# Kernel optimization log

Measured on AMD Instinct MI355X. Metric: run time of the kernel, lower is better.

Reference implementation:

```python
import jax, jax.numpy as jnp
import numpy as np

D_PAIR = 128
C = 128
LN_EPS = 1e-5


def _layernorm(x, w, b):
    m = jnp.mean(x, axis=-1, keepdims=True)
    v = jnp.var(x, axis=-1, keepdims=True)
    return (x - m) * jax.lax.rsqrt(v + LN_EPS) * w + b


def setup_inputs() -> dict:
    key = jax.random.key(0)
    ks = jax.random.split(key, 12)
    B, N = 1, 512
    Z_raw = jax.random.normal(ks[0], (B, N, N, D_PAIR), dtype=jnp.float32)
    Z_mask_row = jnp.ones((B, N, N), dtype=jnp.float32)
    s = 1.0 / np.sqrt(D_PAIR)
    return {
        "Z_raw": Z_raw,
        "Z_mask_row": Z_mask_row,
        "ln1_w": jnp.ones((D_PAIR,), jnp.float32),
        "ln1_b": jnp.zeros((D_PAIR,), jnp.float32),
        "lrp_w": jax.random.normal(ks[1], (2 * C, D_PAIR), jnp.float32) * s,
        "lrp_b": jnp.zeros((2 * C,), jnp.float32),
        "gate_w": jax.random.normal(ks[2], (2 * C, D_PAIR), jnp.float32) * (0.02 * s),
        "gate_b": jnp.ones((2 * C,), jnp.float32),
        "og_w": jax.random.normal(ks[3], (D_PAIR, D_PAIR), jnp.float32) * (0.02 * s),
        "og_b": jnp.ones((D_PAIR,), jnp.float32),
        "ln2_w": jnp.ones((C,), jnp.float32),
        "ln2_b": jnp.zeros((C,), jnp.float32),
        "op_w": jax.random.normal(ks[4], (D_PAIR, D_PAIR), jnp.float32) * (0.02 * s),
        "out_bias": jnp.zeros((D_PAIR,), jnp.float32),
    }


def reference(Z_raw, Z_mask_row, ln1_w, ln1_b, lrp_w, lrp_b, gate_w, gate_b,
              og_w, og_b, ln2_w, ln2_b, op_w, out_bias):
    # Stage 1: norm + gated left/right projections (single chunk since CHUNK_SIZE is None)
    z = _layernorm(Z_raw, ln1_w, ln1_b)                      # [B,N,N,d]
    g = jax.nn.sigmoid(z @ gate_w.T + gate_b)                # [B,N,N,2c]
    proj = (z @ lrp_w.T + lrp_b) * Z_mask_row[..., None] * g  # [B,N,N,2c]
    left, right = jnp.split(proj, 2, axis=-1)                # each [B,N,N,c]
    # Outgoing triangle multiplication: p[b,i,j,c] = sum_k left[b,i,k,c] * right[b,j,k,c]
    tri = jnp.einsum("bikc,bjkc->bijc", left, right)         # [B,N,N,c]
    # Stage 2: output gate on the raw matmul result, norm+proj, bias+gate+residual
    go = jax.nn.sigmoid(tri @ og_w.T + og_b)                 # [B,N,N,d]
    z2 = _layernorm(tri, ln2_w, ln2_b) @ op_w.T              # [B,N,N,d]
    # dropout_mask is all-ones in the source; residual is the matmul output tri
    return tri + go * (z2 + out_bias)
```

## Files before the change

kernel.cpp:

```cpp
#include <hip/hip_runtime.h>

#define NN 512
#define NP (NN*NN)
#define LN_EPS 1e-5f

typedef __attribute__((ext_vector_type(8))) short short8;
typedef __attribute__((ext_vector_type(4))) float float4v;

__device__ __forceinline__ short f2bf(float x){
  union { float f; unsigned u; } un; un.f = x;
  unsigned r = un.u + 0x7fffu + ((un.u >> 16) & 1u);
  return (short)(r >> 16);
}
__device__ __forceinline__ float bf2f(short b){
  union { unsigned u; float f; } un; un.u = ((unsigned)(unsigned short)b) << 16;
  return un.f;
}
__device__ __forceinline__ float sigmoidf_(float x){ return 1.f/(1.f+__expf(-x)); }

__global__ __launch_bounds__(256) void prep_kernel(
    const float* __restrict__ lrpw, const float* __restrict__ gatew,
    const float* __restrict__ ogwf, const float* __restrict__ opwf,
    short* __restrict__ Wpack, short* __restrict__ ogw, short* __restrict__ opw)
{
  int idx = blockIdx.x*256 + threadIdx.x;
  if (idx < 512*128){
    int r = idx >> 7, k = idx & 127, cc = r >> 1;
    float v = (r & 1) ? gatew[cc*128+k] : lrpw[cc*128+k];
    Wpack[idx] = f2bf(v);
  } else if (idx < 512*128 + 128*128) {
    int j = idx - 512*128; ogw[j] = f2bf(ogwf[j]);
  } else {
    int j = idx - 512*128 - 128*128; opw[j] = f2bf(opwf[j]);
  }
}

__global__ __launch_bounds__(512) void stage1_kernel(
    const float* __restrict__ Zraw, const float* __restrict__ mask,
    const float* __restrict__ ln1w, const float* __restrict__ ln1b,
    const float* __restrict__ lrpb, const float* __restrict__ gateb,
    const short* __restrict__ Wpack,
    short* __restrict__ left, short* __restrict__ right)
{
  __shared__ float zraw[64][132];
  __shared__ short zb[64][136];
  __shared__ float part[64][8][2];
  __shared__ float stats[64][2];

  const int t = threadIdx.x;
  const int pos0 = blockIdx.x * 64;

  const float* Zr = Zraw + (size_t)pos0 * 128;
  #pragma unroll
  for (int i = 0; i < 4; i++) {
    int idx = i*512 + t;
    float4v v = *(const float4v*)(Zr + (size_t)idx*4);
    int row = idx >> 5, col = (idx & 31) << 2;
    *(float4v*)&zraw[row][col] = v;
  }
  __syncthreads();

  {
    int pos = t >> 3, seg = t & 7;
    float s = 0.f, ss = 0.f;
    #pragma unroll
    for (int i = 0; i < 16; i++){ float v = zraw[pos][seg*16+i]; s += v; ss += v*v; }
    part[pos][seg][0] = s; part[pos][seg][1] = ss;
  }
  __syncthreads();
  if ((t & 7) == 0) {
    int pos = t >> 3;
    float S = 0.f, SS = 0.f;
    #pragma unroll
    for (int j = 0; j < 8; j++){ S += part[pos][j][0]; SS += part[pos][j][1]; }
    float m = S * (1.f/128.f);
    float v = SS * (1.f/128.f) - m*m;
    stats[pos][0] = m; stats[pos][1] = rsqrtf(v + LN_EPS);
  }
  __syncthreads();
  {
    int pos = t >> 3, seg = t & 7;
    float m = stats[pos][0], r = stats[pos][1];
    #pragma unroll
    for (int i = 0; i < 16; i++){
      int c = seg*16 + i;
      float v = (zraw[pos][c]-m)*r*ln1w[c] + ln1b[c];
      zb[pos][c] = f2bf(v);
    }
  }
  __syncthreads();

  const int w = t >> 6, lane = t & 63;
  const int q = lane >> 4, m15 = lane & 15;

  float4v acc[4][4];
  #pragma unroll
  for (int a = 0; a < 4; a++)
    #pragma unroll
    for (int b = 0; b < 4; b++) acc[a][b] = (float4v){0.f,0.f,0.f,0.f};

  #pragma unroll
  for (int s = 0; s < 4; s++){
    short8 af[4], bfv[4];
    #pragma unroll
    for (int rt = 0; rt < 4; rt++)
      af[rt] = *(const short8*)(Wpack + ((size_t)(w*64 + rt*16 + m15))*128 + s*32 + q*8);
    #pragma unroll
    for (int pt = 0; pt < 4; pt++)
      bfv[pt] = *(const short8*)(&zb[pt*16 + m15][s*32 + q*8]);
    #pragma unroll
    for (int rt = 0; rt < 4; rt++)
      #pragma unroll
      for (int pt = 0; pt < 4; pt++)
        acc[rt][pt] = __builtin_amdgcn_mfma_f32_16x16x32_bf16(af[rt], bfv[pt], acc[rt][pt], 0, 0, 0);
  }

  #pragma unroll
  for (int rt = 0; rt < 4; rt++){
    int rowbase = w*64 + rt*16 + 4*q;
    #pragma unroll
    for (int pt = 0; pt < 4; pt++){
      int pos = pos0 + pt*16 + m15;
      float mk = mask[pos];
      #pragma unroll
      for (int p = 0; p < 2; p++){
        int ch = (rowbase >> 1) + p;
        float lr = acc[rt][pt][2*p]   + lrpb[ch];
        float gt = acc[rt][pt][2*p+1] + gateb[ch];
        float val = lr * mk * sigmoidf_(gt);
        short* dst = (ch < 128) ? (left + (size_t)ch*NP + pos)
                                : (right + (size_t)(ch-128)*NP + pos);
        *dst = f2bf(val);
      }
    }
  }
}

__global__ __launch_bounds__(256) void tri_kernel(
    const short* __restrict__ left, const short* __restrict__ right,
    float* __restrict__ tri)
{
  __shared__ short As[128][72];
  __shared__ short Bs[128][72];

  const int t  = threadIdx.x;
  const int c  = blockIdx.z;
  const int i0 = blockIdx.y * 128;
  const int j0 = blockIdx.x * 128;

  const short* Lp = left  + (size_t)c*NP + (size_t)i0*NN;
  const short* Rp = right + (size_t)c*NP + (size_t)j0*NN;

  const int w = t >> 6, lane = t & 63;
  const int q = lane >> 4, m15 = lane & 15;
  const int wi = w >> 1, wj = w & 1;

  float4v acc[4][4];
  #pragma unroll
  for (int a = 0; a < 4; a++)
    #pragma unroll
    for (int b = 0; b < 4; b++) acc[a][b] = (float4v){0.f,0.f,0.f,0.f};

  for (int it = 0; it < 8; it++){
    const int k0 = it * 64;
    __syncthreads();
    #pragma unroll
    for (int i = 0; i < 4; i++){
      int idx = i*256 + t;
      int row = idx >> 3, c8 = (idx & 7) * 8;
      *(short8*)&As[row][c8] = *(const short8*)(Lp + (size_t)row*NN + k0 + c8);
      *(short8*)&Bs[row][c8] = *(const short8*)(Rp + (size_t)row*NN + k0 + c8);
    }
    __syncthreads();
    #pragma unroll
    for (int s = 0; s < 2; s++){
      short8 af[4], bfv[4];
      #pragma unroll
      for (int mi = 0; mi < 4; mi++)
        af[mi] = *(const short8*)(&As[wi*64 + mi*16 + m15][s*32 + q*8]);
      #pragma unroll
      for (int nj = 0; nj < 4; nj++)
        bfv[nj] = *(const short8*)(&Bs[wj*64 + nj*16 + m15][s*32 + q*8]);
      #pragma unroll
      for (int mi = 0; mi < 4; mi++)
        #pragma unroll
        for (int nj = 0; nj < 4; nj++)
          acc[mi][nj] = __builtin_amdgcn_mfma_f32_16x16x32_bf16(af[mi], bfv[nj], acc[mi][nj], 0, 0, 0);
    }
  }

  float* Tp = tri + (size_t)c*NP;
  #pragma unroll
  for (int mi = 0; mi < 4; mi++)
    #pragma unroll
    for (int nj = 0; nj < 4; nj++)
      #pragma unroll
      for (int r = 0; r < 4; r++){
        int i = i0 + wi*64 + mi*16 + 4*q + r;
        int j = j0 + wj*64 + nj*16 + m15;
        Tp[(size_t)i*NN + j] = acc[mi][nj][r];
      }
}

__global__ __launch_bounds__(256) void stage2_kernel(
    const float* __restrict__ tri,
    const short* __restrict__ ogw, const short* __restrict__ opw,
    const float* __restrict__ ogb, const float* __restrict__ ln2w,
    const float* __restrict__ ln2b, const float* __restrict__ outb,
    float* __restrict__ out)
{
  __shared__ short tb[64][136];
  __shared__ short lnb_s[64][136];
  __shared__ float part[64][4][2];
  __shared__ float stats[64][2];

  const int t = threadIdx.x;
  const int pos0 = blockIdx.x * 64;

  #pragma unroll
  for (int i = 0; i < 8; i++){
    int idx = i*256 + t;
    int cc = idx >> 4, p4 = (idx & 15) << 2;
    float4v v = *(const float4v*)(tri + (size_t)cc*NP + pos0 + p4);
    #pragma unroll
    for (int u = 0; u < 4; u++) tb[p4+u][cc] = f2bf(v[u]);
  }
  __syncthreads();

  {
    int pos = t >> 2, seg = t & 3;
    float s = 0.f, ss = 0.f;
    #pragma unroll
    for (int i = 0; i < 32; i++){ float v = bf2f(tb[pos][seg*32+i]); s += v; ss += v*v; }
    part[pos][seg][0] = s; part[pos][seg][1] = ss;
  }
  __syncthreads();
  if ((t & 3) == 0){
    int pos = t >> 2;
    float S = 0.f, SS = 0.f;
    #pragma unroll
    for (int j = 0; j < 4; j++){ S += part[pos][j][0]; SS += part[pos][j][1]; }
    float m = S * (1.f/128.f);
    float v = SS * (1.f/128.f) - m*m;
    stats[pos][0] = m; stats[pos][1] = rsqrtf(v + LN_EPS);
  }
  __syncthreads();
  {
    int pos = t >> 2, seg = t & 3;
    float m = stats[pos][0], r = stats[pos][1];
    #pragma unroll
    for (int i = 0; i < 32; i++){
      int c = seg*32 + i;
      float v = bf2f(tb[pos][c]);
      lnb_s[pos][c] = f2bf((v-m)*r*ln2w[c] + ln2b[c]);
    }
  }
  __syncthreads();

  const int w = t >> 6, lane = t & 63;
  const int q = lane >> 4, m15 = lane & 15;

  float4v a1[2][4], a2[2][4];
  #pragma unroll
  for (int a = 0; a < 2; a++)
    #pragma unroll
    for (int b = 0; b < 4; b++){ a1[a][b] = (float4v){0.f,0.f,0.f,0.f}; a2[a][b] = (float4v){0.f,0.f,0.f,0.f}; }

  #pragma unroll
  for (int s = 0; s < 4; s++){
    short8 af1[4], af2[4], bv1[2], bv2[2];
    #pragma unroll
    for (int pt = 0; pt < 4; pt++){
      af1[pt] = *(const short8*)(&tb[pt*16 + m15][s*32 + q*8]);
      af2[pt] = *(const short8*)(&lnb_s[pt*16 + m15][s*32 + q*8]);
    }
    #pragma unroll
    for (int dt = 0; dt < 2; dt++){
      int d = w*32 + dt*16 + m15;
      bv1[dt] = *(const short8*)(ogw + (size_t)d*128 + s*32 + q*8);
      bv2[dt] = *(const short8*)(opw + (size_t)d*128 + s*32 + q*8);
    }
    #pragma unroll
    for (int dt = 0; dt < 2; dt++)
      #pragma unroll
      for (int pt = 0; pt < 4; pt++){
        a1[dt][pt] = __builtin_amdgcn_mfma_f32_16x16x32_bf16(af1[pt], bv1[dt], a1[dt][pt], 0, 0, 0);
        a2[dt][pt] = __builtin_amdgcn_mfma_f32_16x16x32_bf16(af2[pt], bv2[dt], a2[dt][pt], 0, 0, 0);
      }
  }

  #pragma unroll
  for (int dt = 0; dt < 2; dt++){
    int d = w*32 + dt*16 + m15;
    float ob = ogb[d], xb = outb[d];
    #pragma unroll
    for (int pt = 0; pt < 4; pt++)
      #pragma unroll
      for (int r = 0; r < 4; r++){
        int pos = pt*16 + 4*q + r;
        float trv = bf2f(tb[pos][d]);
        float go = sigmoidf_(a1[dt][pt][r] + ob);
        float z2 = a2[dt][pt][r] + xb;
        out[(size_t)(pos0+pos)*128 + d] = trv + go*z2;
      }
  }
}

extern "C" void kernel_launch(void* const* d_in, const int* in_sizes, int n_in,
                              void* d_out, int out_size, void* d_ws, size_t ws_size,
                              hipStream_t stream)
{
  const float* Zraw = (const float*)d_in[0];
  const float* mask = (const float*)d_in[1];
  const float* ln1w = (const float*)d_in[2];
  const float* ln1b = (const float*)d_in[3];
  const float* lrpw = (const float*)d_in[4];
  const float* lrpb = (const float*)d_in[5];
  const float* gatew= (const float*)d_in[6];
  const float* gateb= (const float*)d_in[7];
  const float* ogwf = (const float*)d_in[8];
  const float* ogb  = (const float*)d_in[9];
  const float* ln2w = (const float*)d_in[10];
  const float* ln2b = (const float*)d_in[11];
  const float* opwf = (const float*)d_in[12];
  const float* outb = (const float*)d_in[13];
  float* out = (float*)d_out;

  short* left  = (short*)d_ws;
  short* right = left + (size_t)128*NP;
  float* tri   = (float*)(right + (size_t)128*NP);
  short* Wpack = (short*)(tri + (size_t)128*NP);
  short* ogw   = Wpack + 512*128;
  short* opw   = ogw + 128*128;

  hipLaunchKernelGGL(prep_kernel, dim3(384), dim3(256), 0, stream,
                     lrpw, gatew, ogwf, opwf, Wpack, ogw, opw);
  hipLaunchKernelGGL(stage1_kernel, dim3(NP/64), dim3(512), 0, stream,
                     Zraw, mask, ln1w, ln1b, lrpb, gateb, Wpack, left, right);
  hipLaunchKernelGGL(tri_kernel, dim3(4, 4, 128), dim3(256), 0, stream,
                     left, right, tri);
  hipLaunchKernelGGL(stage2_kernel, dim3(NP/64), dim3(256), 0, stream,
                     tri, ogw, opw, ogb, ln2w, ln2b, outb, out);
}
```

Measured before the change: 538.0 us.

## Store tri in bf16, use direct global-to-LDS loads, and register-based layernorms

The triangle matmul output is now stored as bf16 instead of fp32, which halves the write traffic in tri_kernel and the read traffic in stage2. tri_kernel fills shared memory with global_load_lds and an XOR-swizzled layout in place of padding plus register staging. Both layernorms are restructured: stage1 computes its stats in registers with shuffle reductions, and stage2 reads tri per position and reduces through a small shared array, which cuts barriers and shared-memory round trips. The stage2 path already used bf16 for tri, so the extra rounding in storage is minor.

```diff
diff --git a/kernel.cpp b/kernel.cpp
--- a/kernel.cpp
+++ b/kernel.cpp
@@ -17,6 +17,11 @@
   return un.f;
 }
 __device__ __forceinline__ float sigmoidf_(float x){ return 1.f/(1.f+__expf(-x)); }
+
+__device__ __forceinline__ void gl2lds16(const short* g, short* l){
+  __builtin_amdgcn_global_load_lds((const __attribute__((address_space(1))) void*)g,
+                                   (__attribute__((address_space(3))) void*)l, 16, 0, 0);
+}
 
 __global__ __launch_bounds__(256) void prep_kernel(
     const float* __restrict__ lrpw, const float* __restrict__ gatew,
@@ -42,52 +47,43 @@
     const short* __restrict__ Wpack,
     short* __restrict__ left, short* __restrict__ right)
 {
-  __shared__ float zraw[64][132];
   __shared__ short zb[64][136];
-  __shared__ float part[64][8][2];
-  __shared__ float stats[64][2];
 
   const int t = threadIdx.x;
   const int pos0 = blockIdx.x * 64;
-
-  const float* Zr = Zraw + (size_t)pos0 * 128;
-  #pragma unroll
-  for (int i = 0; i < 4; i++) {
-    int idx = i*512 + t;
-    float4v v = *(const float4v*)(Zr + (size_t)idx*4);
-    int row = idx >> 5, col = (idx & 31) << 2;
-    *(float4v*)&zraw[row][col] = v;
-  }
-  __syncthreads();
-
-  {
-    int pos = t >> 3, seg = t & 7;
-    float s = 0.f, ss = 0.f;
-    #pragma unroll
-    for (int i = 0; i < 16; i++){ float v = zraw[pos][seg*16+i]; s += v; ss += v*v; }
-    part[pos][seg][0] = s; part[pos][seg][1] = ss;
-  }
-  __syncthreads();
-  if ((t & 7) == 0) {
-    int pos = t >> 3;
-    float S = 0.f, SS = 0.f;
-    #pragma unroll
-    for (int j = 0; j < 8; j++){ S += part[pos][j][0]; SS += part[pos][j][1]; }
-    float m = S * (1.f/128.f);
-    float v = SS * (1.f/128.f) - m*m;
-    stats[pos][0] = m; stats[pos][1] = rsqrtf(v + LN_EPS);
-  }
-  __syncthreads();
-  {
-    int pos = t >> 3, seg = t & 7;
-    float m = stats[pos][0], r = stats[pos][1];
-    #pragma unroll
-    for (int i = 0; i < 16; i++){
-      int c = seg*16 + i;
-      float v = (zraw[pos][c]-m)*r*ln1w[c] + ln1b[c];
-      zb[pos][c] = f2bf(v);
-    }
-  }
+  const int pos = t >> 3, seg = t & 7;
+
+  const float* zp = Zraw + (size_t)(pos0 + pos)*128 + seg*16;
+  float x[16];
+  #pragma unroll
+  for (int i = 0; i < 4; i++){
+    float4v v = *(const float4v*)(zp + i*4);
+    x[4*i] = v[0]; x[4*i+1] = v[1]; x[4*i+2] = v[2]; x[4*i+3] = v[3];
+  }
+  float s = 0.f, ss = 0.f;
+  #pragma unroll
+  for (int i = 0; i < 16; i++){ s += x[i]; ss += x[i]*x[i]; }
+  #pragma unroll
+  for (int off = 1; off < 8; off <<= 1){
+    s  += __shfl_xor(s,  off);
+    ss += __shfl_xor(ss, off);
+  }
+  float m = s * (1.f/128.f);
+  float r = rsqrtf(ss * (1.f/128.f) - m*m + LN_EPS);
+
+  short8 o0, o1;
+  #pragma unroll
+  for (int i = 0; i < 8; i++){
+    int c = seg*16 + i;
+    o0[i] = f2bf((x[i]-m)*r*ln1w[c] + ln1b[c]);
+  }
+  #pragma unroll
+  for (int i = 0; i < 8; i++){
+    int c = seg*16 + 8 + i;
+    o1[i] = f2bf((x[8+i]-m)*r*ln1w[c] + ln1b[c]);
+  }
+  *(short8*)&zb[pos][seg*16]     = o0;
+  *(short8*)&zb[pos][seg*16 + 8] = o1;
   __syncthreads();
 
   const int w = t >> 6, lane = t & 63;
@@ -100,14 +96,14 @@
     for (int b = 0; b < 4; b++) acc[a][b] = (float4v){0.f,0.f,0.f,0.f};
 
   #pragma unroll
-  for (int s = 0; s < 4; s++){
+  for (int sstep = 0; sstep < 4; sstep++){
     short8 af[4], bfv[4];
     #pragma unroll
     for (int rt = 0; rt < 4; rt++)
-      af[rt] = *(const short8*)(Wpack + ((size_t)(w*64 + rt*16 + m15))*128 + s*32 + q*8);
+      af[rt] = *(const short8*)(Wpack + ((size_t)(w*64 + rt*16 + m15))*128 + sstep*32 + q*8);
     #pragma unroll
     for (int pt = 0; pt < 4; pt++)
-      bfv[pt] = *(const short8*)(&zb[pt*16 + m15][s*32 + q*8]);
+      bfv[pt] = *(const short8*)(&zb[pt*16 + m15][sstep*32 + q*8]);
     #pragma unroll
     for (int rt = 0; rt < 4; rt++)
       #pragma unroll
@@ -120,16 +116,16 @@
     int rowbase = w*64 + rt*16 + 4*q;
     #pragma unroll
     for (int pt = 0; pt < 4; pt++){
-      int pos = pos0 + pt*16 + m15;
-      float mk = mask[pos];
+      int posj = pos0 + pt*16 + m15;
+      float mk = mask[posj];
       #pragma unroll
       for (int p = 0; p < 2; p++){
         int ch = (rowbase >> 1) + p;
         float lr = acc[rt][pt][2*p]   + lrpb[ch];
         float gt = acc[rt][pt][2*p+1] + gateb[ch];
         float val = lr * mk * sigmoidf_(gt);
-        short* dst = (ch < 128) ? (left + (size_t)ch*NP + pos)
-                                : (right + (size_t)(ch-128)*NP + pos);
+        short* dst = (ch < 128) ? (left + (size_t)ch*NP + posj)
+                                : (right + (size_t)(ch-128)*NP + posj);
         *dst = f2bf(val);
       }
     }
@@ -138,23 +134,25 @@
 
 __global__ __launch_bounds__(256) void tri_kernel(
     const short* __restrict__ left, const short* __restrict__ right,
-    float* __restrict__ tri)
-{
-  __shared__ short As[128][72];
-  __shared__ short Bs[128][72];
+    short* __restrict__ tri_bf)
+{
+  __shared__ short As[128][64];
+  __shared__ short Bs[128][64];
 
   const int t  = threadIdx.x;
   const int c  = blockIdx.z;
   const int i0 = blockIdx.y * 128;
   const int j0 = blockIdx.x * 128;
 
-  const short* Lp = left  + (size_t)c*NP + (size_t)i0*NN;
-  const short* Rp = right + (size_t)c*NP + (size_t)j0*NN;
-
   const int w = t >> 6, lane = t & 63;
   const int q = lane >> 4, m15 = lane & 15;
   const int wi = w >> 1, wj = w & 1;
 
+  const int lrow = lane >> 3;
+  const int lu   = (lane & 7) ^ lrow;
+  const short* Lsrc = left  + (size_t)c*NP + (size_t)(i0 + w*32 + lrow)*NN + lu*8;
+  const short* Rsrc = right + (size_t)c*NP + (size_t)(j0 + w*32 + lrow)*NN + lu*8;
+
   float4v acc[4][4];
   #pragma unroll
   for (int a = 0; a < 4; a++)
@@ -166,10 +164,8 @@
     __syncthreads();
     #pragma unroll
     for (int i = 0; i < 4; i++){
-      int idx = i*256 + t;
-      int row = idx >> 3, c8 = (idx & 7) * 8;
-      *(short8*)&As[row][c8] = *(const short8*)(Lp + (size_t)row*NN + k0 + c8);
-      *(short8*)&Bs[row][c8] = *(const short8*)(Rp + (size_t)row*NN + k0 + c8);
+      gl2lds16(Lsrc + (size_t)i*8*NN + k0, &As[w*32 + i*8][0]);
+      gl2lds16(Rsrc + (size_t)i*8*NN + k0, &Bs[w*32 + i*8][0]);
     }
     __syncthreads();
     #pragma unroll
@@ -177,10 +173,10 @@
       short8 af[4], bfv[4];
       #pragma unroll
       for (int mi = 0; mi < 4; mi++)
-        af[mi] = *(const short8*)(&As[wi*64 + mi*16 + m15][s*32 + q*8]);
+        af[mi] = *(const short8*)(&As[wi*64 + mi*16 + m15][((s*4 + q) ^ (m15 & 7))*8]);
       #pragma unroll
       for (int nj = 0; nj < 4; nj++)
-        bfv[nj] = *(const short8*)(&Bs[wj*64 + nj*16 + m15][s*32 + q*8]);
+        bfv[nj] = *(const short8*)(&Bs[wj*64 + nj*16 + m15][((s*4 + q) ^ (m15 & 7))*8]);
       #pragma unroll
       for (int mi = 0; mi < 4; mi++)
         #pragma unroll
@@ -189,7 +185,7 @@
     }
   }
 
-  float* Tp = tri + (size_t)c*NP;
+  short* Tp = tri_bf + (size_t)c*NP;
   #pragma unroll
   for (int mi = 0; mi < 4; mi++)
     #pragma unroll
@@ -198,12 +194,12 @@
       for (int r = 0; r < 4; r++){
         int i = i0 + wi*64 + mi*16 + 4*q + r;
         int j = j0 + wj*64 + nj*16 + m15;
-        Tp[(size_t)i*NN + j] = acc[mi][nj][r];
+        Tp[(size_t)i*NN + j] = f2bf(acc[mi][nj][r]);
       }
 }
 
 __global__ __launch_bounds__(256) void stage2_kernel(
-    const float* __restrict__ tri,
+    const short* __restrict__ tri_bf,
     const short* __restrict__ ogw, const short* __restrict__ opw,
     const float* __restrict__ ogb, const float* __restrict__ ln2w,
     const float* __restrict__ ln2b, const float* __restrict__ outb,
@@ -211,53 +207,49 @@
 {
   __shared__ short tb[64][136];
   __shared__ short lnb_s[64][136];
-  __shared__ float part[64][4][2];
-  __shared__ float stats[64][2];
+  __shared__ float part[64][9];
 
   const int t = threadIdx.x;
   const int pos0 = blockIdx.x * 64;
-
-  #pragma unroll
-  for (int i = 0; i < 8; i++){
-    int idx = i*256 + t;
-    int cc = idx >> 4, p4 = (idx & 15) << 2;
-    float4v v = *(const float4v*)(tri + (size_t)cc*NP + pos0 + p4);
-    #pragma unroll
-    for (int u = 0; u < 4; u++) tb[p4+u][cc] = f2bf(v[u]);
-  }
+  const int lane = t & 63, w = t >> 6;
+
+  short8 pk[4];
+  float s = 0.f, ss = 0.f;
+  #pragma unroll
+  for (int u = 0; u < 4; u++){
+    short8 p;
+    #pragma unroll
+    for (int j = 0; j < 8; j++){
+      int cc = w*32 + u*8 + j;
+      short b = tri_bf[(size_t)cc*NP + pos0 + lane];
+      p[j] = b;
+      float v = bf2f(b); s += v; ss += v*v;
+    }
+    pk[u] = p;
+    *(short8*)&tb[lane][w*32 + u*8] = p;
+  }
+  part[lane][2*w]   = s;
+  part[lane][2*w+1] = ss;
   __syncthreads();
 
-  {
-    int pos = t >> 2, seg = t & 3;
-    float s = 0.f, ss = 0.f;
-    #pragma unroll
-    for (int i = 0; i < 32; i++){ float v = bf2f(tb[pos][seg*32+i]); s += v; ss += v*v; }
-    part[pos][seg][0] = s; part[pos][seg][1] = ss;
+  float S = 0.f, SS = 0.f;
+  #pragma unroll
+  for (int j = 0; j < 4; j++){ S += part[lane][2*j]; SS += part[lane][2*j+1]; }
+  float m = S * (1.f/128.f);
+  float r = rsqrtf(SS * (1.f/128.f) - m*m + LN_EPS);
+  #pragma unroll
+  for (int u = 0; u < 4; u++){
+    short8 p = pk[u], o;
+    #pragma unroll
+    for (int j = 0; j < 8; j++){
+      int cc = w*32 + u*8 + j;
+      float v = bf2f(p[j]);
+      o[j] = f2bf((v - m)*r*ln2w[cc] + ln2b[cc]);
+    }
+    *(short8*)&lnb_s[lane][w*32 + u*8] = o;
   }
   __syncthreads();
-  if ((t & 3) == 0){
-    int pos = t >> 2;
-    float S = 0.f, SS = 0.f;
-    #pragma unroll
-    for (int j = 0; j < 4; j++){ S += part[pos][j][0]; SS += part[pos][j][1]; }
-    float m = S * (1.f/128.f);
-    float v = SS * (1.f/128.f) - m*m;
-    stats[pos][0] = m; stats[pos][1] = rsqrtf(v + LN_EPS);
-  }
-  __syncthreads();
-  {
-    int pos = t >> 2, seg = t & 3;
-    float m = stats[pos][0], r = stats[pos][1];
-    #pragma unroll
-    for (int i = 0; i < 32; i++){
-      int c = seg*32 + i;
-      float v = bf2f(tb[pos][c]);
-      lnb_s[pos][c] = f2bf((v-m)*r*ln2w[c] + ln2b[c]);
-    }
-  }
-  __syncthreads();
-
-  const int w = t >> 6, lane = t & 63;
+
   const int q = lane >> 4, m15 = lane & 15;
 
   float4v a1[2][4], a2[2][4];
@@ -267,18 +259,18 @@
     for (int b = 0; b < 4; b++){ a1[a][b] = (float4v){0.f,0.f,0.f,0.f}; a2[a][b] = (float4v){0.f,0.f,0.f,0.f}; }
 
   #pragma unroll
-  for (int s = 0; s < 4; s++){
+  for (int sstep = 0; sstep < 4; sstep++){
     short8 af1[4], af2[4], bv1[2], bv2[2];
     #pragma unroll
     for (int pt = 0; pt < 4; pt++){
-      af1[pt] = *(const short8*)(&tb[pt*16 + m15][s*32 + q*8]);
-      af2[pt] = *(const short8*)(&lnb_s[pt*16 + m15][s*32 + q*8]);
+      af1[pt] = *(const short8*)(&tb[pt*16 + m15][sstep*32 + q*8]);
+      af2[pt] = *(const short8*)(&lnb_s[pt*16 + m15][sstep*32 + q*8]);
     }
     #pragma unroll
     for (int dt = 0; dt < 2; dt++){
       int d = w*32 + dt*16 + m15;
-      bv1[dt] = *(const short8*)(ogw + (size_t)d*128 + s*32 + q*8);
-      bv2[dt] = *(const short8*)(opw + (size_t)d*128 + s*32 + q*8);
+      bv1[dt] = *(const short8*)(ogw + (size_t)d*128 + sstep*32 + q*8);
+      bv2[dt] = *(const short8*)(opw + (size_t)d*128 + sstep*32 + q*8);
     }
     #pragma unroll
     for (int dt = 0; dt < 2; dt++)
@@ -296,11 +288,11 @@
     #pragma unroll
     for (int pt = 0; pt < 4; pt++)
       #pragma unroll
-      for (int r = 0; r < 4; r++){
-        int pos = pt*16 + 4*q + r;
+      for (int r2 = 0; r2 < 4; r2++){
+        int pos = pt*16 + 4*q + r2;
         float trv = bf2f(tb[pos][d]);
-        float go = sigmoidf_(a1[dt][pt][r] + ob);
-        float z2 = a2[dt][pt][r] + xb;
+        float go = sigmoidf_(a1[dt][pt][r2] + ob);
+        float z2 = a2[dt][pt][r2] + xb;
         out[(size_t)(pos0+pos)*128 + d] = trv + go*z2;
       }
   }
@@ -326,19 +318,19 @@
   const float* outb = (const float*)d_in[13];
   float* out = (float*)d_out;
 
-  short* left  = (short*)d_ws;
-  short* right = left + (size_t)128*NP;
-  float* tri   = (float*)(right + (size_t)128*NP);
-  short* Wpack = (short*)(tri + (size_t)128*NP);
-  short* ogw   = Wpack + 512*128;
-  short* opw   = ogw + 128*128;
+  short* left   = (short*)d_ws;
+  short* right  = left + (size_t)128*NP;
+  short* tri_bf = right + (size_t)128*NP;
+  short* Wpack  = tri_bf + (size_t)128*NP;
+  short* ogw    = Wpack + 512*128;
+  short* opw    = ogw + 128*128;
 
   hipLaunchKernelGGL(prep_kernel, dim3(384), dim3(256), 0, stream,
                      lrpw, gatew, ogwf, opwf, Wpack, ogw, opw);
   hipLaunchKernelGGL(stage1_kernel, dim3(NP/64), dim3(512), 0, stream,
                      Zraw, mask, ln1w, ln1b, lrpb, gateb, Wpack, left, right);
   hipLaunchKernelGGL(tri_kernel, dim3(4, 4, 128), dim3(256), 0, stream,
-                     left, right, tri);
+                     left, right, tri_bf);
   hipLaunchKernelGGL(stage2_kernel, dim3(NP/64), dim3(256), 0, stream,
-                     tri, ogw, opw, ogb, ln2w, ln2b, outb, out);
-}
+                     tri_bf, ogw, opw, ogb, ln2w, ln2b, outb, out);
+}
```

New measurement: 460.5 us. -14.4%, faster.
